# Kernel tuning notes

Measured on AMD Instinct MI355X. Metric: run time of the kernel, lower is better.

The kernel has to match this reference:

```python
import jax, jax.numpy as jnp
import numpy as np

C = 256
CQK = C // 8  # 32

def setup_inputs() -> dict:
    key = jax.random.key(0)
    ks = jax.random.split(key, 9)
    B, H, W = 4, 64, 64
    shp = (B, C, H, W)
    v = jax.random.normal(ks[0], shp, dtype=jnp.float32)
    k = jax.random.normal(ks[1], shp, dtype=jnp.float32)
    q = jax.random.normal(ks[2], shp, dtype=jnp.float32)
    s = 1.0 / np.sqrt(C)
    Wq = jax.random.normal(ks[3], (CQK, C), dtype=jnp.float32) * s
    bq = jnp.zeros((CQK,), dtype=jnp.float32)
    Wk = jax.random.normal(ks[4], (CQK, C), dtype=jnp.float32) * s
    bk = jnp.zeros((CQK,), dtype=jnp.float32)
    Wv = jax.random.normal(ks[5], (C, C), dtype=jnp.float32) * s
    bv = jnp.zeros((C,), dtype=jnp.float32)
    # torch inits gamma=0 (out == v); use small nonzero so attention path is exercised
    gamma = jnp.full((1,), 0.5, dtype=jnp.float32)
    return {"v": v, "k": k, "q": q, "Wq": Wq, "bq": bq, "Wk": Wk, "bk": bk,
            "Wv": Wv, "bv": bv, "gamma": gamma}

def reference(v, k, q, Wq, bq, Wk, bk, Wv, bv, gamma):
    B, Cc, Hh, Ww = v.shape
    N = Hh * Ww
    # 1x1 convs == per-pixel channel matmuls
    pq = jnp.einsum('oc,bchw->bohw', Wq, q) + bq[None, :, None, None]  # B,CQK,H,W
    pk = jnp.einsum('oc,bchw->bohw', Wk, k) + bk[None, :, None, None]
    pv = jnp.einsum('oc,bchw->bohw', Wv, v) + bv[None, :, None, None]  # B,C,H,W
    pq = pq.reshape(B, -1, N)  # B,d,N
    pk = pk.reshape(B, -1, N)
    pv = pv.reshape(B, Cc, N)
    # energy[b,n,m] = <q_n, k_m>; softmax over m (keys)
    energy = jnp.einsum('bdn,bdm->bnm', pq, pk)
    attn = jax.nn.softmax(energy, axis=-1)
    # out[b,c,n] = sum_m v[b,c,m] * attn[b,n,m]
    out = jnp.einsum('bcm,bnm->bcn', pv, attn).reshape(B, Cc, Hh, Ww)
    return gamma * out + v
```

## Files before the change

kernel.cpp:

```cpp
#include <hip/hip_runtime.h>
#include <hip/hip_bf16.h>

typedef __attribute__((ext_vector_type(8))) short short8_t;
typedef __attribute__((ext_vector_type(4))) short short4_t;
typedef __attribute__((ext_vector_type(4))) unsigned short ushort4_t;
typedef __attribute__((ext_vector_type(4))) float float4_t;

#define B_   4
#define C_   256
#define N_   4096
#define DQK  32
#define LOG2E 1.4426950408889634f

#define VMCNT4   asm volatile("s_waitcnt vmcnt(4)" ::: "memory")
#define LGKM0    asm volatile("s_waitcnt lgkmcnt(0)" ::: "memory")
#define SBAR     __builtin_amdgcn_s_barrier()
#define SCHEDB   __builtin_amdgcn_sched_barrier(0)

__device__ __forceinline__ unsigned short f2bf(float x) {
    union { float f; unsigned int u; } v; v.f = x;
    unsigned int r = v.u + 0x7FFFu + ((v.u >> 16) & 1u);
    return (unsigned short)(r >> 16);
}
__device__ __forceinline__ unsigned short f2bf_hw(float x) {
    return __bfloat16_as_ushort(__float2bfloat16(x));
}
__device__ __forceinline__ float bf2f(unsigned short u) {
    union { unsigned int u; float f; } v; v.u = ((unsigned int)u) << 16; return v.f;
}

__global__ __launch_bounds__(256) void cast_w_k(
        const float* __restrict__ Wq, const float* __restrict__ Wk,
        const float* __restrict__ Wv,
        unsigned short* __restrict__ Wqb, unsigned short* __restrict__ Wkb,
        unsigned short* __restrict__ Wvb) {
    int i = blockIdx.x * 256 + threadIdx.x;
    if (i < 8192)            Wqb[i] = f2bf(Wq[i]);
    else if (i < 16384)      Wkb[i - 8192] = f2bf(Wk[i - 8192]);
    else                     Wvb[i - 16384] = f2bf(Wv[i - 16384]);
}

__global__ __launch_bounds__(256) void proj_qk_k(
        const float* __restrict__ q_in, const float* __restrict__ k_in,
        const unsigned short* __restrict__ Wqb, const unsigned short* __restrict__ Wkb,
        const float* __restrict__ bq, const float* __restrict__ bk,
        unsigned short* __restrict__ pqT, unsigned short* __restrict__ pkT) {
    int b = blockIdx.y, z = blockIdx.z;
    const float* X = z ? k_in : q_in;
    const unsigned short* W = z ? Wkb : Wqb;
    const float* bias = z ? bk : bq;
    unsigned short* P = z ? pkT : pqT;
    float scl = z ? 1.0f : LOG2E;
    int tid = threadIdx.x, wave = tid >> 6, lane = tid & 63, l15 = lane & 15, g = lane >> 4;
    int nb = blockIdx.x * 64 + wave * 16;
    float4_t acc0 = {0.f, 0.f, 0.f, 0.f}, acc1 = {0.f, 0.f, 0.f, 0.f};
    const float* Xcol = X + (size_t)b * C_ * N_ + nb + l15;
#pragma unroll
    for (int kk = 0; kk < 8; ++kk) {
        short8_t a;
#pragma unroll
        for (int j = 0; j < 8; ++j)
            a[j] = (short)f2bf(Xcol[(size_t)(kk * 32 + 8 * g + j) * N_]);
        short8_t b0 = *(const short8_t*)(W + (size_t)l15 * C_ + kk * 32 + 8 * g);
        short8_t b1 = *(const short8_t*)(W + (size_t)(16 + l15) * C_ + kk * 32 + 8 * g);
        acc0 = __builtin_amdgcn_mfma_f32_16x16x32_bf16(a, b0, acc0, 0, 0, 0);
        acc1 = __builtin_amdgcn_mfma_f32_16x16x32_bf16(a, b1, acc1, 0, 0, 0);
    }
#pragma unroll
    for (int r = 0; r < 4; ++r) {
        int n = nb + 4 * g + r;
        P[((size_t)b * N_ + n) * DQK + l15]      = f2bf((acc0[r] + bias[l15]) * scl);
        P[((size_t)b * N_ + n) * DQK + 16 + l15] = f2bf((acc1[r] + bias[16 + l15]) * scl);
    }
}

__global__ __launch_bounds__(256) void proj_v_k(
        const float* __restrict__ v_in, const unsigned short* __restrict__ Wvb,
        const float* __restrict__ bv, unsigned short* __restrict__ pv) {
    int b = blockIdx.y;
    int tid = threadIdx.x, wave = tid >> 6, lane = tid & 63, l15 = lane & 15, g = lane >> 4;
    int mb = blockIdx.x * 16;
    int m = mb + l15;
    int k32 = m & 31;
    int pcol = (k32 < 16) ? ((k32 >> 2) * 8 + (k32 & 3))
                          : (((k32 - 16) >> 2) * 8 + 4 + (k32 & 3));
    int mcol = (m & ~31) + pcol;
    float4_t acc[4];
#pragma unroll
    for (int i = 0; i < 4; ++i) acc[i] = (float4_t){0.f, 0.f, 0.f, 0.f};
    const float* Vcol = v_in + (size_t)b * C_ * N_ + mb + l15;
#pragma unroll
    for (int kk = 0; kk < 8; ++kk) {
        short8_t bf;
#pragma unroll
        for (int j = 0; j < 8; ++j)
            bf[j] = (short)f2bf(Vcol[(size_t)(kk * 32 + 8 * g + j) * N_]);
#pragma unroll
        for (int ct = 0; ct < 4; ++ct) {
            short8_t af = *(const short8_t*)(Wvb + (size_t)(wave * 64 + ct * 16 + l15) * C_ + kk * 32 + 8 * g);
            acc[ct] = __builtin_amdgcn_mfma_f32_16x16x32_bf16(af, bf, acc[ct], 0, 0, 0);
        }
    }
#pragma unroll
    for (int ct = 0; ct < 4; ++ct)
#pragma unroll
        for (int r = 0; r < 4; ++r) {
            int c = wave * 64 + ct * 16 + 4 * g + r;
            pv[((size_t)b * C_ + c) * N_ + mcol] = f2bf(acc[ct][r] + bv[c]);
        }
}

__global__ __launch_bounds__(256, 2) void attn_split_k(
        const unsigned short* __restrict__ pqT, const unsigned short* __restrict__ pkT,
        const unsigned short* __restrict__ pv,
        unsigned short* __restrict__ accP, float* __restrict__ lP, int KS) {
    __shared__ __align__(16) unsigned short VT[256][64];
    __shared__ __align__(16) short8_t Pl[2][4][2][4][16];
    int nqb = gridDim.x;
    int lin = blockIdx.x + nqb * (blockIdx.y + KS * blockIdx.z);
    int cpx = (nqb * KS * 4) >> 3;
    int sl  = (lin & 7) * cpx + (lin >> 3);
    int qbi = sl % nqb;
    int s   = (sl / nqb) % KS;
    int b   = sl / (nqb * KS);

    int kps = N_ / KS, ks0 = s * kps, nt = kps >> 6;
    int tid = threadIdx.x, wave = tid >> 6, lane = tid & 63, l15 = lane & 15, g = lane >> 4;
    int qb = qbi * 64;
    int sw = (l15 & 7) << 4;
    int rl = lane >> 3, cl = (lane & 7) ^ rl;

    short8_t qf = *(const short8_t*)(pqT + ((size_t)b * N_ + qb + wave * 16 + l15) * DQK + 8 * g);
    float4_t acc[4][4];
#pragma unroll
    for (int i = 0; i < 4; ++i)
#pragma unroll
        for (int j = 0; j < 4; ++j) acc[i][j] = (float4_t){0.f, 0.f, 0.f, 0.f};
    float4_t accl = {0.f, 0.f, 0.f, 0.f};
    short8_t onef;
#pragma unroll
    for (int j = 0; j < 8; ++j) onef[j] = (short)0x3F80;
    const float4_t zero4 = {0.f, 0.f, 0.f, 0.f};
    const char* pvb8 = (const char*)(pv + (size_t)b * C_ * N_);
    const char* pkTb = (const char*)pkT + (size_t)b * N_ * DQK * 2;

    unsigned soff[8];
#pragma unroll
    for (int i = 0; i < 8; ++i)
        soff[i] = (unsigned)(((wave * 64 + i * 8 + rl) * N_ + ks0 + 8 * cl) * 2);
    unsigned koff = (unsigned)(((ks0 + l15) * DQK + 8 * g) * 2);
    const char* vbA = (const char*)&VT[0][0] + (wave * 64 + l15) * 128 + ((16 * g) ^ sw);
    const char* vbB = (const char*)&VT[0][0] + (wave * 64 + l15) * 128 + ((64 + 16 * g) ^ sw);

#define STAGE()                                                               \
    _Pragma("unroll")                                                         \
    for (int i_ = 0; i_ < 8; ++i_) {                                          \
        __builtin_amdgcn_global_load_lds(                                     \
            (const __attribute__((address_space(1))) unsigned int*)(const void*)(pvb8 + soff[i_]), \
            (__attribute__((address_space(3))) unsigned int*)(void*)&VT[wave * 64 + i_ * 8][0], 16, 0, 0); \
        soff[i_] += 128;                                                      \
    }

#define KFLOAD(DST)                                                           \
    _Pragma("unroll")                                                         \
    for (int it_ = 0; it_ < 4; ++it_)                                         \
        DST[it_] = *(const short8_t*)(pkTb + koff + it_ * 1024);              \
    koff += 4096;

#define VREAD(DST)                                                            \
    _Pragma("unroll")                                                         \
    for (int ct_ = 0; ct_ < 4; ++ct_) {                                       \
        DST[ct_][0] = *(const short8_t*)(vbA + ct_ * 2048);                   \
        DST[ct_][1] = *(const short8_t*)(vbB + ct_ * 2048);                   \
    }

#define PFREAD(DST, CB)                                                       \
    _Pragma("unroll")                                                         \
    for (int qt_ = 0; qt_ < 4; ++qt_)                                         \
        _Pragma("unroll")                                                     \
        for (int kh_ = 0; kh_ < 2; ++kh_)                                     \
            DST[qt_][kh_] = Pl[CB][qt_][kh_][g][l15];

#define QKWR(KF, NB)                                                          \
    {                                                                          \
        float4_t sv_[4];                                                       \
        _Pragma("unroll")                                                      \
        for (int it_ = 0; it_ < 4; ++it_)                                      \
            sv_[it_] = __builtin_amdgcn_mfma_f32_16x16x32_bf16(KF[it_], qf, zero4, 0, 0, 0); \
        float p_[16];                                                          \
        _Pragma("unroll")                                                      \
        for (int it_ = 0; it_ < 4; ++it_)                                      \
            _Pragma("unroll")                                                  \
            for (int r_ = 0; r_ < 4; ++r_)                                     \
                p_[it_ * 4 + r_] = exp2f(sv_[it_][r_]);                        \
        short8_t pbn0_, pbn1_;                                                 \
        _Pragma("unroll")                                                      \
        for (int j_ = 0; j_ < 4; ++j_) {                                       \
            pbn0_[j_]     = (short)f2bf_hw(p_[j_]);                            \
            pbn0_[4 + j_] = (short)f2bf_hw(p_[4 + j_]);                        \
            pbn1_[j_]     = (short)f2bf_hw(p_[8 + j_]);                        \
            pbn1_[4 + j_] = (short)f2bf_hw(p_[12 + j_]);                       \
        }                                                                      \
        accl = __builtin_amdgcn_mfma_f32_16x16x32_bf16(onef, pbn0_, accl, 0, 0, 0); \
        accl = __builtin_amdgcn_mfma_f32_16x16x32_bf16(onef, pbn1_, accl, 0, 0, 0); \
        Pl[NB][wave][0][g][l15] = pbn0_;                                       \
        Pl[NB][wave][1][g][l15] = pbn1_;                                       \
    }

#define PVM_ALL(VF, PF)                                                       \
    _Pragma("unroll")                                                         \
    for (int ct_ = 0; ct_ < 4; ++ct_)                                         \
        _Pragma("unroll")                                                     \
        for (int qt_ = 0; qt_ < 4; ++qt_) {                                   \
            acc[ct_][qt_] = __builtin_amdgcn_mfma_f32_16x16x32_bf16(VF[ct_][0], PF[qt_][0], acc[ct_][qt_], 0, 0, 0); \
            acc[ct_][qt_] = __builtin_amdgcn_mfma_f32_16x16x32_bf16(VF[ct_][1], PF[qt_][1], acc[ct_][qt_], 0, 0, 0); \
        }

#define BODY(T, KFC, KFN, CB, NB)                                             \
    {                                                                          \
        VMCNT4; SCHEDB;                                                        \
        short8_t vf_[4][2], pf_[4][2];                                         \
        VREAD(vf_)                                                             \
        PFREAD(pf_, CB)                                                        \
        LGKM0; SCHEDB;                                                         \
        if ((T) + 1 < nt) { STAGE() KFLOAD(KFN) }                              \
        __builtin_amdgcn_s_setprio(1);                                         \
        PVM_ALL(vf_, pf_)                                                      \
        __builtin_amdgcn_s_setprio(0);                                         \
        if ((T) + 1 < nt) { QKWR(KFC, NB) }                                    \
        LGKM0; SCHEDB;                                                         \
        SBAR;                                                                  \
    }

    short8_t kfA[4], kfB[4];
    STAGE()
    KFLOAD(kfA)
    KFLOAD(kfB)
    QKWR(kfA, 0)
    LGKM0; SCHEDB;
    SBAR;

    for (int t = 0; t < nt; t += 2) {
        BODY(t,     kfB, kfA, 0, 1)
        BODY(t + 1, kfA, kfB, 1, 0)
    }

    if (g == 0)
        lP[(size_t)(b * KS + s) * N_ + qb + wave * 16 + l15] = accl[0];
    unsigned short* accOut = accP + ((size_t)(b * KS + s) * C_) * N_;
#pragma unroll
    for (int ct = 0; ct < 4; ++ct)
#pragma unroll
        for (int qt = 0; qt < 4; ++qt)
#pragma unroll
            for (int r = 0; r < 4; ++r) {
                int c = wave * 64 + ct * 16 + 4 * g + r;
                accOut[(size_t)c * N_ + qb + qt * 16 + l15] = f2bf_hw(acc[ct][qt][r]);
            }
#undef STAGE
#undef KFLOAD
#undef VREAD
#undef PFREAD
#undef QKWR
#undef PVM_ALL
#undef BODY
}

__global__ __launch_bounds__(256) void combine_k(
        const unsigned short* __restrict__ accP, const float* __restrict__ lP,
        const float* __restrict__ v_in, const float* __restrict__ gamma,
        float* __restrict__ out, int KS) {
    int i = blockIdx.x * 256 + threadIdx.x;
    const int nq4 = N_ / 4;
    int q0 = (i % nq4) * 4;
    int c  = (i / nq4) % C_;
    int b  = i / (nq4 * C_);
    float4_t num = {0.f, 0.f, 0.f, 0.f}, den = {0.f, 0.f, 0.f, 0.f};
    for (int s = 0; s < KS; ++s) {
        float4_t l4 = *(const float4_t*)(lP + (size_t)(b * KS + s) * N_ + q0);
        ushort4_t a4 = *(const ushort4_t*)(accP + ((size_t)(b * KS + s) * C_ + c) * N_ + q0);
#pragma unroll
        for (int j = 0; j < 4; ++j) {
            den[j] += l4[j];
            num[j] += bf2f(a4[j]);
        }
    }
    float gm = gamma[0];
    size_t idx = ((size_t)(b * C_ + c)) * N_ + q0;
    float4_t vi = *(const float4_t*)(v_in + idx);
    float4_t o;
#pragma unroll
    for (int j = 0; j < 4; ++j) o[j] = gm * num[j] / den[j] + vi[j];
    *(float4_t*)(out + idx) = o;
}

extern "C" void kernel_launch(void* const* d_in, const int* in_sizes, int n_in,
                              void* d_out, int out_size, void* d_ws, size_t ws_size,
                              hipStream_t stream) {
    (void)in_sizes; (void)n_in; (void)out_size;
    const float* v_in  = (const float*)d_in[0];
    const float* k_in  = (const float*)d_in[1];
    const float* q_in  = (const float*)d_in[2];
    const float* Wq    = (const float*)d_in[3];
    const float* bq    = (const float*)d_in[4];
    const float* Wk    = (const float*)d_in[5];
    const float* bk    = (const float*)d_in[6];
    const float* Wv    = (const float*)d_in[7];
    const float* bv    = (const float*)d_in[8];
    const float* gamma = (const float*)d_in[9];
    float* out = (float*)d_out;

    char* ws = (char*)d_ws;
    unsigned short* pvb = (unsigned short*)(ws + 0);
    unsigned short* pqT = (unsigned short*)(ws + 8388608);
    unsigned short* pkT = (unsigned short*)(ws + 9437184);
    unsigned short* Wqb = (unsigned short*)(ws + 10502144);
    unsigned short* Wkb = (unsigned short*)(ws + 10518528);
    unsigned short* Wvb = (unsigned short*)(ws + 10534912);
    const size_t base2 = 10665984;

    int KS = 4;
    while (KS > 1) {
        size_t need = base2 + (size_t)KS * 8388608 + (size_t)KS * 65536;
        if (need <= ws_size) break;
        KS >>= 1;
    }
    unsigned short* accP = (unsigned short*)(ws + base2);
    float* lP = (float*)(ws + base2 + (size_t)KS * 8388608);

    cast_w_k<<<320, 256, 0, stream>>>(Wq, Wk, Wv, Wqb, Wkb, Wvb);
    proj_qk_k<<<dim3(64, 4, 2), 256, 0, stream>>>(q_in, k_in, Wqb, Wkb, bq, bk, pqT, pkT);
    proj_v_k<<<dim3(256, 4), 256, 0, stream>>>(v_in, Wvb, bv, pvb);
    attn_split_k<<<dim3(64, KS, 4), 256, 0, stream>>>(pqT, pkT, pvb, accP, lP, KS);
    combine_k<<<4096, 256, 0, stream>>>(accP, lP, v_in, gamma, out, KS);
}
```

Baseline: 101.8 us.

## Load V fragments directly to registers with double-buffered global loads, halve key splits

Drops the LDS staging of the V tile via global_load_lds and instead loads V MFMA fragments straight into registers with inline-asm global_load_dwordx4, double-buffering both V and K fragments across iterations under explicit vmcnt waits. This removes LDS traffic and the swizzled LDS reads for V, at the cost of more registers in flight and uncoalesced per-lane global reads. The split-K factor drops from 4 to 2, halving the partial buffers and combine work but also halving the attention grid. Workspace offsets are shifted, with padding added after pv.

```diff
diff --git a/kernel.cpp b/kernel.cpp
--- a/kernel.cpp
+++ b/kernel.cpp
@@ -2,7 +2,6 @@
 #include <hip/hip_bf16.h>
 
 typedef __attribute__((ext_vector_type(8))) short short8_t;
-typedef __attribute__((ext_vector_type(4))) short short4_t;
 typedef __attribute__((ext_vector_type(4))) unsigned short ushort4_t;
 typedef __attribute__((ext_vector_type(4))) float float4_t;
 
@@ -12,7 +11,9 @@
 #define DQK  32
 #define LOG2E 1.4426950408889634f
 
-#define VMCNT4   asm volatile("s_waitcnt vmcnt(4)" ::: "memory")
+#define VMCNT12  asm volatile("s_waitcnt vmcnt(12)" ::: "memory")
+#define VMCNT20  asm volatile("s_waitcnt vmcnt(20)" ::: "memory")
+#define VMCNT0   asm volatile("s_waitcnt vmcnt(0)" ::: "memory")
 #define LGKM0    asm volatile("s_waitcnt lgkmcnt(0)" ::: "memory")
 #define SBAR     __builtin_amdgcn_s_barrier()
 #define SCHEDB   __builtin_amdgcn_sched_barrier(0)
@@ -114,7 +115,6 @@
         const unsigned short* __restrict__ pqT, const unsigned short* __restrict__ pkT,
         const unsigned short* __restrict__ pv,
         unsigned short* __restrict__ accP, float* __restrict__ lP, int KS) {
-    __shared__ __align__(16) unsigned short VT[256][64];
     __shared__ __align__(16) short8_t Pl[2][4][2][4][16];
     int nqb = gridDim.x;
     int lin = blockIdx.x + nqb * (blockIdx.y + KS * blockIdx.z);
@@ -127,8 +127,6 @@
     int kps = N_ / KS, ks0 = s * kps, nt = kps >> 6;
     int tid = threadIdx.x, wave = tid >> 6, lane = tid & 63, l15 = lane & 15, g = lane >> 4;
     int qb = qbi * 64;
-    int sw = (l15 & 7) << 4;
-    int rl = lane >> 3, cl = (lane & 7) ^ rl;
 
     short8_t qf = *(const short8_t*)(pqT + ((size_t)b * N_ + qb + wave * 16 + l15) * DQK + 8 * g);
     float4_t acc[4][4];
@@ -144,35 +142,30 @@
     const char* pvb8 = (const char*)(pv + (size_t)b * C_ * N_);
     const char* pkTb = (const char*)pkT + (size_t)b * N_ * DQK * 2;
 
-    unsigned soff[8];
-#pragma unroll
-    for (int i = 0; i < 8; ++i)
-        soff[i] = (unsigned)(((wave * 64 + i * 8 + rl) * N_ + ks0 + 8 * cl) * 2);
+    unsigned voff[4];
+#pragma unroll
+    for (int ct = 0; ct < 4; ++ct)
+        voff[ct] = (unsigned)((((wave * 64 + ct * 16 + l15) * N_) + ks0 + 8 * g) * 2);
     unsigned koff = (unsigned)(((ks0 + l15) * DQK + 8 * g) * 2);
-    const char* vbA = (const char*)&VT[0][0] + (wave * 64 + l15) * 128 + ((16 * g) ^ sw);
-    const char* vbB = (const char*)&VT[0][0] + (wave * 64 + l15) * 128 + ((64 + 16 * g) ^ sw);
-
-#define STAGE()                                                               \
-    _Pragma("unroll")                                                         \
-    for (int i_ = 0; i_ < 8; ++i_) {                                          \
-        __builtin_amdgcn_global_load_lds(                                     \
-            (const __attribute__((address_space(1))) unsigned int*)(const void*)(pvb8 + soff[i_]), \
-            (__attribute__((address_space(3))) unsigned int*)(void*)&VT[wave * 64 + i_ * 8][0], 16, 0, 0); \
-        soff[i_] += 128;                                                      \
-    }
-
-#define KFLOAD(DST)                                                           \
-    _Pragma("unroll")                                                         \
-    for (int it_ = 0; it_ < 4; ++it_)                                         \
-        DST[it_] = *(const short8_t*)(pkTb + koff + it_ * 1024);              \
-    koff += 4096;
-
-#define VREAD(DST)                                                            \
+
+#define GLDI(DST, OFF, BASE, IMM)                                             \
+    asm volatile("global_load_dwordx4 %0, %1, %2 offset:" IMM                 \
+                 : "=v"(DST) : "v"(OFF), "s"(BASE));
+
+#define VLOAD(DST)                                                            \
     _Pragma("unroll")                                                         \
     for (int ct_ = 0; ct_ < 4; ++ct_) {                                       \
-        DST[ct_][0] = *(const short8_t*)(vbA + ct_ * 2048);                   \
-        DST[ct_][1] = *(const short8_t*)(vbB + ct_ * 2048);                   \
-    }
+        GLDI(DST[ct_][0], voff[ct_], pvb8, "0")                               \
+        GLDI(DST[ct_][1], voff[ct_], pvb8, "64")                              \
+        voff[ct_] += 128;                                                     \
+    }
+
+#define KFLOAD(DST)                                                           \
+    GLDI(DST[0], koff, pkTb, "0")                                             \
+    GLDI(DST[1], koff, pkTb, "1024")                                          \
+    GLDI(DST[2], koff, pkTb, "2048")                                          \
+    GLDI(DST[3], koff, pkTb, "3072")                                          \
+    koff += 4096;
 
 #define PFREAD(DST, CB)                                                       \
     _Pragma("unroll")                                                         \
@@ -216,34 +209,37 @@
             acc[ct_][qt_] = __builtin_amdgcn_mfma_f32_16x16x32_bf16(VF[ct_][1], PF[qt_][1], acc[ct_][qt_], 0, 0, 0); \
         }
 
-#define BODY(T, KFC, KFN, CB, NB)                                             \
+#define BODY(T, VC, KC, CB, NB)                                               \
     {                                                                          \
-        VMCNT4; SCHEDB;                                                        \
-        short8_t vf_[4][2], pf_[4][2];                                         \
-        VREAD(vf_)                                                             \
+        short8_t pf_[4][2];                                                    \
         PFREAD(pf_, CB)                                                        \
-        LGKM0; SCHEDB;                                                         \
-        if ((T) + 1 < nt) { STAGE() KFLOAD(KFN) }                              \
+        VMCNT12; SCHEDB;                                                       \
         __builtin_amdgcn_s_setprio(1);                                         \
-        PVM_ALL(vf_, pf_)                                                      \
+        PVM_ALL(VC, pf_)                                                       \
         __builtin_amdgcn_s_setprio(0);                                         \
-        if ((T) + 1 < nt) { QKWR(KFC, NB) }                                    \
+        VLOAD(VC)                                                              \
+        if ((T) + 1 < nt) { QKWR(KC, NB) }                                     \
+        KFLOAD(KC)                                                             \
         LGKM0; SCHEDB;                                                         \
         SBAR;                                                                  \
     }
 
-    short8_t kfA[4], kfB[4];
-    STAGE()
+    short8_t vX[4][2], vY[4][2], kfA[4], kfB[4];
+    KFLOAD(kfB)
+    VLOAD(vX)
     KFLOAD(kfA)
+    VLOAD(vY)
+    VMCNT20; SCHEDB;
+    QKWR(kfB, 0)
     KFLOAD(kfB)
-    QKWR(kfA, 0)
     LGKM0; SCHEDB;
     SBAR;
 
     for (int t = 0; t < nt; t += 2) {
-        BODY(t,     kfB, kfA, 0, 1)
-        BODY(t + 1, kfA, kfB, 1, 0)
-    }
+        BODY(t,     vX, kfA, 0, 1)
+        BODY(t + 1, vY, kfB, 1, 0)
+    }
+    VMCNT0;
 
     if (g == 0)
         lP[(size_t)(b * KS + s) * N_ + qb + wave * 16 + l15] = accl[0];
@@ -257,9 +253,9 @@
                 int c = wave * 64 + ct * 16 + 4 * g + r;
                 accOut[(size_t)c * N_ + qb + qt * 16 + l15] = f2bf_hw(acc[ct][qt][r]);
             }
-#undef STAGE
+#undef GLDI
+#undef VLOAD
 #undef KFLOAD
-#undef VREAD
 #undef PFREAD
 #undef QKWR
 #undef PVM_ALL
@@ -312,14 +308,14 @@
 
     char* ws = (char*)d_ws;
     unsigned short* pvb = (unsigned short*)(ws + 0);
-    unsigned short* pqT = (unsigned short*)(ws + 8388608);
-    unsigned short* pkT = (unsigned short*)(ws + 9437184);
-    unsigned short* Wqb = (unsigned short*)(ws + 10502144);
-    unsigned short* Wkb = (unsigned short*)(ws + 10518528);
-    unsigned short* Wvb = (unsigned short*)(ws + 10534912);
-    const size_t base2 = 10665984;
-
-    int KS = 4;
+    unsigned short* pqT = (unsigned short*)(ws + 8404992);
+    unsigned short* pkT = (unsigned short*)(ws + 9453568);
+    unsigned short* Wqb = (unsigned short*)(ws + 10526720);
+    unsigned short* Wkb = (unsigned short*)(ws + 10543104);
+    unsigned short* Wvb = (unsigned short*)(ws + 10559488);
+    const size_t base2 = 10690560;
+
+    int KS = 2;
     while (KS > 1) {
         size_t need = base2 + (size_t)KS * 8388608 + (size_t)KS * 65536;
         if (need <= ws_size) break;
```

Result: slower. 126.4 us (+24.2%).

## Split attention block into 8 waves with producer waves computing softmax probabilities

Applied to the files above, without the earlier changes.

The attention kernel goes from 256 to 512 threads. Each wave now owns 32 output channels instead of 64, and only the first four waves compute QK scores, exp and bf16 P tiles, which all waves then read from LDS. The row-sum is now a plain float add followed by a shuffle reduction, replacing the MFMA-with-ones trick, and the key split drops from 4 to 2. This halves per-wave accumulator registers and spreads the PV matmul across more waves. In exchange the softmax work becomes imbalanced across waves, and there are fewer blocks in the grid.

```diff
diff --git a/kernel.cpp b/kernel.cpp
--- a/kernel.cpp
+++ b/kernel.cpp
@@ -2,7 +2,6 @@
 #include <hip/hip_bf16.h>
 
 typedef __attribute__((ext_vector_type(8))) short short8_t;
-typedef __attribute__((ext_vector_type(4))) short short4_t;
 typedef __attribute__((ext_vector_type(4))) unsigned short ushort4_t;
 typedef __attribute__((ext_vector_type(4))) float float4_t;
 
@@ -13,6 +12,7 @@
 #define LOG2E 1.4426950408889634f
 
 #define VMCNT4   asm volatile("s_waitcnt vmcnt(4)" ::: "memory")
+#define VMCNT0   asm volatile("s_waitcnt vmcnt(0)" ::: "memory")
 #define LGKM0    asm volatile("s_waitcnt lgkmcnt(0)" ::: "memory")
 #define SBAR     __builtin_amdgcn_s_barrier()
 #define SCHEDB   __builtin_amdgcn_sched_barrier(0)
@@ -110,7 +110,7 @@
         }
 }
 
-__global__ __launch_bounds__(256, 2) void attn_split_k(
+__global__ __launch_bounds__(512, 4) void attn_split_k(
         const unsigned short* __restrict__ pqT, const unsigned short* __restrict__ pkT,
         const unsigned short* __restrict__ pv,
         unsigned short* __restrict__ accP, float* __restrict__ lP, int KS) {
@@ -127,134 +127,149 @@
     int kps = N_ / KS, ks0 = s * kps, nt = kps >> 6;
     int tid = threadIdx.x, wave = tid >> 6, lane = tid & 63, l15 = lane & 15, g = lane >> 4;
     int qb = qbi * 64;
+    bool prod = wave < 4;
+    int qs = wave & 3;
+    int rl = lane >> 3, cl = (lane & 7) ^ rl;
     int sw = (l15 & 7) << 4;
-    int rl = lane >> 3, cl = (lane & 7) ^ rl;
-
-    short8_t qf = *(const short8_t*)(pqT + ((size_t)b * N_ + qb + wave * 16 + l15) * DQK + 8 * g);
-    float4_t acc[4][4];
-#pragma unroll
-    for (int i = 0; i < 4; ++i)
+
+    short8_t qf = *(const short8_t*)(pqT + ((size_t)b * N_ + qb + qs * 16 + l15) * DQK + 8 * g);
+    float4_t acc[2][4];
+#pragma unroll
+    for (int i = 0; i < 2; ++i)
 #pragma unroll
         for (int j = 0; j < 4; ++j) acc[i][j] = (float4_t){0.f, 0.f, 0.f, 0.f};
-    float4_t accl = {0.f, 0.f, 0.f, 0.f};
-    short8_t onef;
-#pragma unroll
-    for (int j = 0; j < 8; ++j) onef[j] = (short)0x3F80;
+    float l_acc = 0.f;
     const float4_t zero4 = {0.f, 0.f, 0.f, 0.f};
     const char* pvb8 = (const char*)(pv + (size_t)b * C_ * N_);
     const char* pkTb = (const char*)pkT + (size_t)b * N_ * DQK * 2;
 
-    unsigned soff[8];
-#pragma unroll
-    for (int i = 0; i < 8; ++i)
-        soff[i] = (unsigned)(((wave * 64 + i * 8 + rl) * N_ + ks0 + 8 * cl) * 2);
+    unsigned soff[4];
+#pragma unroll
+    for (int i = 0; i < 4; ++i)
+        soff[i] = (unsigned)(((wave * 32 + i * 8 + rl) * N_ + ks0 + 8 * cl) * 2);
     unsigned koff = (unsigned)(((ks0 + l15) * DQK + 8 * g) * 2);
-    const char* vbA = (const char*)&VT[0][0] + (wave * 64 + l15) * 128 + ((16 * g) ^ sw);
-    const char* vbB = (const char*)&VT[0][0] + (wave * 64 + l15) * 128 + ((64 + 16 * g) ^ sw);
+    const char* vbA = (const char*)&VT[0][0] + (wave * 32 + l15) * 128 + ((16 * g) ^ sw);
+    const char* vbB = (const char*)&VT[0][0] + (wave * 32 + l15) * 128 + ((64 + 16 * g) ^ sw);
+    char* PlB = (char*)&Pl[0][0][0][0][0];
+    const char* prd = PlB + g * 256 + l15 * 16;
+    char* pwr = PlB + qs * 2048 + g * 256 + l15 * 16;
+
+    short8_t kf[4];
 
 #define STAGE()                                                               \
     _Pragma("unroll")                                                         \
-    for (int i_ = 0; i_ < 8; ++i_) {                                          \
+    for (int i_ = 0; i_ < 4; ++i_) {                                          \
         __builtin_amdgcn_global_load_lds(                                     \
             (const __attribute__((address_space(1))) unsigned int*)(const void*)(pvb8 + soff[i_]), \
-            (__attribute__((address_space(3))) unsigned int*)(void*)&VT[wave * 64 + i_ * 8][0], 16, 0, 0); \
+            (__attribute__((address_space(3))) unsigned int*)(void*)((char*)&VT[0][0] + (wave * 32 + i_ * 8) * 128), \
+            16, 0, 0);                                                        \
         soff[i_] += 128;                                                      \
     }
 
-#define KFLOAD(DST)                                                           \
+#define KFLOAD()                                                              \
     _Pragma("unroll")                                                         \
     for (int it_ = 0; it_ < 4; ++it_)                                         \
-        DST[it_] = *(const short8_t*)(pkTb + koff + it_ * 1024);              \
+        kf[it_] = *(const short8_t*)(pkTb + koff + it_ * 1024);               \
     koff += 4096;
 
 #define VREAD(DST)                                                            \
     _Pragma("unroll")                                                         \
-    for (int ct_ = 0; ct_ < 4; ++ct_) {                                       \
+    for (int ct_ = 0; ct_ < 2; ++ct_) {                                       \
         DST[ct_][0] = *(const short8_t*)(vbA + ct_ * 2048);                   \
         DST[ct_][1] = *(const short8_t*)(vbB + ct_ * 2048);                   \
     }
 
-#define PFREAD(DST, CB)                                                       \
+#define PFREAD(DST, CBOFF)                                                    \
     _Pragma("unroll")                                                         \
     for (int qt_ = 0; qt_ < 4; ++qt_)                                         \
         _Pragma("unroll")                                                     \
         for (int kh_ = 0; kh_ < 2; ++kh_)                                     \
-            DST[qt_][kh_] = Pl[CB][qt_][kh_][g][l15];
-
-#define QKWR(KF, NB)                                                          \
+            DST[qt_][kh_] = *(const short8_t*)(prd + (CBOFF) + qt_ * 2048 + kh_ * 1024);
+
+#define QKWR(NBOFF)                                                           \
     {                                                                          \
         float4_t sv_[4];                                                       \
         _Pragma("unroll")                                                      \
         for (int it_ = 0; it_ < 4; ++it_)                                      \
-            sv_[it_] = __builtin_amdgcn_mfma_f32_16x16x32_bf16(KF[it_], qf, zero4, 0, 0, 0); \
+            sv_[it_] = __builtin_amdgcn_mfma_f32_16x16x32_bf16(kf[it_], qf, zero4, 0, 0, 0); \
         float p_[16];                                                          \
         _Pragma("unroll")                                                      \
         for (int it_ = 0; it_ < 4; ++it_)                                      \
             _Pragma("unroll")                                                  \
             for (int r_ = 0; r_ < 4; ++r_)                                     \
                 p_[it_ * 4 + r_] = exp2f(sv_[it_][r_]);                        \
-        short8_t pbn0_, pbn1_;                                                 \
+        l_acc += ((p_[0] + p_[1]) + (p_[2] + p_[3])) + ((p_[4] + p_[5]) + (p_[6] + p_[7])) \
+               + ((p_[8] + p_[9]) + (p_[10] + p_[11])) + ((p_[12] + p_[13]) + (p_[14] + p_[15])); \
+        short8_t pb0_, pb1_;                                                   \
         _Pragma("unroll")                                                      \
         for (int j_ = 0; j_ < 4; ++j_) {                                       \
-            pbn0_[j_]     = (short)f2bf_hw(p_[j_]);                            \
-            pbn0_[4 + j_] = (short)f2bf_hw(p_[4 + j_]);                        \
-            pbn1_[j_]     = (short)f2bf_hw(p_[8 + j_]);                        \
-            pbn1_[4 + j_] = (short)f2bf_hw(p_[12 + j_]);                       \
+            pb0_[j_]     = (short)f2bf_hw(p_[j_]);                             \
+            pb0_[4 + j_] = (short)f2bf_hw(p_[4 + j_]);                         \
+            pb1_[j_]     = (short)f2bf_hw(p_[8 + j_]);                         \
+            pb1_[4 + j_] = (short)f2bf_hw(p_[12 + j_]);                        \
         }                                                                      \
-        accl = __builtin_amdgcn_mfma_f32_16x16x32_bf16(onef, pbn0_, accl, 0, 0, 0); \
-        accl = __builtin_amdgcn_mfma_f32_16x16x32_bf16(onef, pbn1_, accl, 0, 0, 0); \
-        Pl[NB][wave][0][g][l15] = pbn0_;                                       \
-        Pl[NB][wave][1][g][l15] = pbn1_;                                       \
-    }
-
-#define PVM_ALL(VF, PF)                                                       \
-    _Pragma("unroll")                                                         \
-    for (int ct_ = 0; ct_ < 4; ++ct_)                                         \
+        *(short8_t*)(pwr + (NBOFF))        = pb0_;                             \
+        *(short8_t*)(pwr + (NBOFF) + 1024) = pb1_;                             \
+    }
+
+#define PVM(VF, PF)                                                           \
+    _Pragma("unroll")                                                         \
+    for (int ct_ = 0; ct_ < 2; ++ct_)                                         \
         _Pragma("unroll")                                                     \
         for (int qt_ = 0; qt_ < 4; ++qt_) {                                   \
             acc[ct_][qt_] = __builtin_amdgcn_mfma_f32_16x16x32_bf16(VF[ct_][0], PF[qt_][0], acc[ct_][qt_], 0, 0, 0); \
             acc[ct_][qt_] = __builtin_amdgcn_mfma_f32_16x16x32_bf16(VF[ct_][1], PF[qt_][1], acc[ct_][qt_], 0, 0, 0); \
         }
 
-#define BODY(T, KFC, KFN, CB, NB)                                             \
+#define BODY(T, CBOFF, NBOFF)                                                 \
     {                                                                          \
-        VMCNT4; SCHEDB;                                                        \
-        short8_t vf_[4][2], pf_[4][2];                                         \
+        if (prod) { VMCNT4; } else { VMCNT0; }                                 \
+        SCHEDB;                                                                \
+        short8_t vf_[2][2], pf_[4][2];                                         \
         VREAD(vf_)                                                             \
-        PFREAD(pf_, CB)                                                        \
+        PFREAD(pf_, CBOFF)                                                     \
         LGKM0; SCHEDB;                                                         \
-        if ((T) + 1 < nt) { STAGE() KFLOAD(KFN) }                              \
+        if ((T) + 1 < nt) {                                                    \
+            STAGE()                                                            \
+            SCHEDB;                                                            \
+            if (prod) { QKWR(NBOFF) KFLOAD() }                                 \
+            SCHEDB;                                                            \
+        }                                                                      \
         __builtin_amdgcn_s_setprio(1);                                         \
-        PVM_ALL(vf_, pf_)                                                      \
+        PVM(vf_, pf_)                                                          \
         __builtin_amdgcn_s_setprio(0);                                         \
-        if ((T) + 1 < nt) { QKWR(KFC, NB) }                                    \
         LGKM0; SCHEDB;                                                         \
         SBAR;                                                                  \
     }
 
-    short8_t kfA[4], kfB[4];
     STAGE()
-    KFLOAD(kfA)
-    KFLOAD(kfB)
-    QKWR(kfA, 0)
+    if (prod) {
+        KFLOAD()
+        QKWR(0)
+        KFLOAD()
+    }
     LGKM0; SCHEDB;
     SBAR;
 
     for (int t = 0; t < nt; t += 2) {
-        BODY(t,     kfB, kfA, 0, 1)
-        BODY(t + 1, kfA, kfB, 1, 0)
-    }
-
-    if (g == 0)
-        lP[(size_t)(b * KS + s) * N_ + qb + wave * 16 + l15] = accl[0];
+        BODY(t,     0, 8192)
+        BODY(t + 1, 8192, 0)
+    }
+
+    if (prod) {
+        l_acc += __shfl_xor(l_acc, 16);
+        l_acc += __shfl_xor(l_acc, 32);
+        if (g == 0)
+            lP[(size_t)(b * KS + s) * N_ + qb + qs * 16 + l15] = l_acc;
+    }
     unsigned short* accOut = accP + ((size_t)(b * KS + s) * C_) * N_;
 #pragma unroll
-    for (int ct = 0; ct < 4; ++ct)
+    for (int ct = 0; ct < 2; ++ct)
 #pragma unroll
         for (int qt = 0; qt < 4; ++qt)
 #pragma unroll
             for (int r = 0; r < 4; ++r) {
-                int c = wave * 64 + ct * 16 + 4 * g + r;
+                int c = wave * 32 + ct * 16 + 4 * g + r;
                 accOut[(size_t)c * N_ + qb + qt * 16 + l15] = f2bf_hw(acc[ct][qt][r]);
             }
 #undef STAGE
@@ -262,7 +277,7 @@
 #undef VREAD
 #undef PFREAD
 #undef QKWR
-#undef PVM_ALL
+#undef PVM
 #undef BODY
 }
 
@@ -312,14 +327,14 @@
 
     char* ws = (char*)d_ws;
     unsigned short* pvb = (unsigned short*)(ws + 0);
-    unsigned short* pqT = (unsigned short*)(ws + 8388608);
-    unsigned short* pkT = (unsigned short*)(ws + 9437184);
-    unsigned short* Wqb = (unsigned short*)(ws + 10502144);
-    unsigned short* Wkb = (unsigned short*)(ws + 10518528);
-    unsigned short* Wvb = (unsigned short*)(ws + 10534912);
-    const size_t base2 = 10665984;
-
-    int KS = 4;
+    unsigned short* pqT = (unsigned short*)(ws + 8404992);
+    unsigned short* pkT = (unsigned short*)(ws + 9453568);
+    unsigned short* Wqb = (unsigned short*)(ws + 10526720);
+    unsigned short* Wkb = (unsigned short*)(ws + 10543104);
+    unsigned short* Wvb = (unsigned short*)(ws + 10559488);
+    const size_t base2 = 10690560;
+
+    int KS = 2;
     while (KS > 1) {
         size_t need = base2 + (size_t)KS * 8388608 + (size_t)KS * 65536;
         if (need <= ws_size) break;
@@ -331,6 +346,6 @@
     cast_w_k<<<320, 256, 0, stream>>>(Wq, Wk, Wv, Wqb, Wkb, Wvb);
     proj_qk_k<<<dim3(64, 4, 2), 256, 0, stream>>>(q_in, k_in, Wqb, Wkb, bq, bk, pqT, pkT);
     proj_v_k<<<dim3(256, 4), 256, 0, stream>>>(v_in, Wvb, bv, pvb);
-    attn_split_k<<<dim3(64, KS, 4), 256, 0, stream>>>(pqT, pkT, pvb, accP, lP, KS);
+    attn_split_k<<<dim3(64, KS, 4), 512, 0, stream>>>(pqT, pkT, pvb, accP, lP, KS);
     combine_k<<<4096, 256, 0, stream>>>(accP, lP, v_in, gamma, out, KS);
 }
```

Measured after the change: 94.86 us, median of 3. 1.07x faster.
